# Performance work log

Hardware: AMD Instinct MI355X
Metric: run time of the kernel (lower is better)

## Reference

```python
import jax, jax.numpy as jnp
import numpy as np

N_NODES, N_EDGES, N_PAIRS, FEAT, N_LAYERS = 10000, 160000, 8, 64, 2


def setup_inputs() -> dict:
    key = jax.random.key(0)
    ks = jax.random.split(key, 12)
    s = 1.0 / np.sqrt(FEAT)
    x = jax.random.normal(ks[0], (N_NODES, FEAT), jnp.float32)
    # distinct node ids so unique(pos) has exactly 2*N_PAIRS elements (static B)
    pos = jax.random.permutation(ks[1], N_NODES)[: 2 * N_PAIRS].reshape(N_PAIRS, 2).astype(jnp.int32)
    edge_src = jax.random.randint(ks[2], (N_EDGES,), 0, N_NODES, jnp.int32)
    edge_dst = jax.random.randint(ks[3], (N_EDGES,), 0, N_NODES, jnp.int32)
    edge_weight = jax.random.uniform(ks[4], (N_EDGES,), jnp.float32)
    f0_w = jax.random.normal(ks[5], (N_LAYERS, FEAT, FEAT), jnp.float32) * s
    f0_b = jax.random.normal(ks[6], (N_LAYERS, FEAT), jnp.float32) * 0.01
    f1_w = jax.random.normal(ks[7], (N_LAYERS, FEAT, FEAT), jnp.float32) * s
    f1_b = jax.random.normal(ks[8], (N_LAYERS, FEAT), jnp.float32) * 0.01
    conv_w = jax.random.normal(ks[9], (N_LAYERS, FEAT, FEAT), jnp.float32) * s
    conv_b = jax.random.normal(ks[10], (N_LAYERS, FEAT), jnp.float32) * 0.01
    return {"x": x, "pos": pos, "edge_src": edge_src, "edge_dst": edge_dst,
            "edge_weight": edge_weight, "f0_w": f0_w, "f0_b": f0_b,
            "f1_w": f1_w, "f1_b": f1_b, "conv_w": conv_w, "conv_b": conv_b}


def reference(x, pos, edge_src, edge_dst, edge_weight, f0_w, f0_b, f1_w, f1_b, conv_w, conv_b):
    N = x.shape[0]
    M = pos.shape[0]
    B = 2 * M  # pos entries are distinct -> B unique labeled nodes (static)
    L = f0_w.shape[0]
    # convert_pos: sel_id = unique labeled nodes, ret = flat index into (B*N)
    sel_id, inv = jnp.unique(pos, return_inverse=True, size=B, fill_value=0)
    inv = inv.reshape(pos.shape)
    ret = pos + inv[:, ::-1] * N  # (M,2): pair (u,v) -> x0[batch_of_v, u], x0[batch_of_u, v]
    idx0 = jnp.arange(B)

    h = x  # layer 0: (N,F); later layers: (B,N,H)
    for i in range(L):
        if i == 0:
            base = h @ f0_w[0] + f0_b[0]                         # (N,H)
            x0 = jnp.broadcast_to(base, (B,) + base.shape)       # (B,N,H)
            x1 = h[sel_id] @ f1_w[0] + f1_b[0]                   # (B,H)
        else:
            x0 = h @ f0_w[i] + f0_b[i]                           # (B,N,H)
            x1 = h[idx0, sel_id] @ f1_w[i] + f1_b[i]             # (B,H)
        x0 = x0.at[idx0, sel_id].set(x1)  # scatter labeled-node embeddings
        # sparse adjacency conv: aggregate over edges, then linear
        xT = jnp.swapaxes(x0, 0, 1)                              # (N,B,H)
        msgs = xT[edge_src] * edge_weight[:, None, None]         # (E,B,H)
        agg = jax.ops.segment_sum(msgs, edge_dst, num_segments=N)  # (N,B,H)
        h = jnp.swapaxes(agg, 0, 1) @ conv_w[i] + conv_b[i]      # (B,N,H)
        if i < L - 1:
            h = jax.nn.relu(h)
    flat = h.reshape(B * N, -1)
    return flat[ret]  # (M, 2, H)
```

## Files before the change

kernel.cpp:

```cpp
#include <hip/hip_runtime.h>

#define F 64
#define SECAP 8192
#define TCAP 2048

__global__ __launch_bounds__(256) void k0_init(const int* __restrict__ pos, int B,
                                               int4* __restrict__ z0, int nz0_vec,
                                               int* __restrict__ sel,
                                               int* __restrict__ slotb,
                                               int* __restrict__ slotn) {
  int bid = blockIdx.x, tid = threadIdx.x;
  int i = bid * 256 + tid;
  if (i < nz0_vec) z0[i] = make_int4(0, 0, 0, 0);
  if (bid == (int)gridDim.x - 1) {
    __shared__ int ps[64];
    if (tid < B) ps[tid] = pos[tid];
    __syncthreads();
    if (tid < B) {
      int v = ps[tid];
      int pv = ps[tid ^ 1];
      int rank = 0, pr = 0;
      for (int j = 0; j < B; ++j) { rank += (ps[j] < v); pr += (ps[j] < pv); }
      sel[rank] = v;
      slotb[tid] = pr;
      slotn[tid] = v;
    }
  }
}

__global__ __launch_bounds__(256) void k23_main(
    const float* __restrict__ x, const float* __restrict__ f0w,
    const float* __restrict__ f0b, float* __restrict__ base0, int N,
    const int* __restrict__ esrc, const int* __restrict__ edst,
    const float* __restrict__ ew, int E, int B,
    const int* __restrict__ sel, const int* __restrict__ slotn,
    int* __restrict__ cnt, int* __restrict__ mark, int* __restrict__ slot_of,
    int* __restrict__ SEb, int* __restrict__ SEd, float* __restrict__ SEw,
    int* __restrict__ TEn, int* __restrict__ TEsrc2, float* __restrict__ TEw2,
    int4* __restrict__ z1, int nz1_vec, int nG, int nE) {
  int bid = blockIdx.x, tid = threadIdx.x;
  if (bid < nG) {
    __shared__ float Wl[64][64];
    __shared__ float xr[4][64];
    int tx = tid & 63, ty = tid >> 6;
    for (int i = tid; i < 4096; i += 256) Wl[i >> 6][i & 63] = f0w[i];
    int row = bid * 4 + ty;
    if (row < N) xr[ty][tx] = x[(size_t)row * F + tx];
    __syncthreads();
    if (row < N) {
      float sum = f0b[tx];
#pragma unroll
      for (int f = 0; f < 64; ++f) sum += xr[ty][f] * Wl[f][tx];
      base0[(size_t)row * F + tx] = sum;
    }
  } else if (bid < nG + nE) {
    int ebi = bid - nG;
    __shared__ int selL[64], tnL[64];
    if (tid < B) { selL[tid] = sel[tid]; tnL[tid] = slotn[tid]; }
    __syncthreads();
    if (ebi == 0 && tid < B) {
      int n = selL[tid];
      int old = atomicAdd(&mark[n], 1);
      if (old == 0) slot_of[n] = atomicAdd(&cnt[2], 1);
    }
    int e = ebi * 256 + tid;
    if (e < E) {
      int s = esrc[e], d = edst[e];
      float w = ew[e];
      int bi = -1, ti = -1;
      for (int i = 0; i < B; ++i) {
        if (s == selL[i]) bi = i;
        if (d == tnL[i]) ti = i;
      }
      if (bi >= 0) {
        int idx = atomicAdd(&cnt[0], 1);
        if (idx < SECAP) { SEb[idx] = bi; SEd[idx] = d; SEw[idx] = w; }
      }
      if (ti >= 0) {
        int idx = atomicAdd(&TEn[ti], 1);
        if (idx < TCAP) { TEsrc2[ti * TCAP + idx] = s; TEw2[ti * TCAP + idx] = w; }
        int old = atomicAdd(&mark[s], 1);
        if (old == 0) slot_of[s] = atomicAdd(&cnt[2], 1);
      }
    }
  } else {
    int i = (bid - nG - nE) * 256 + tid;
    if (i < nz1_vec) z1[i] = make_int4(0, 0, 0, 0);
  }
}

__global__ __launch_bounds__(256) void k4b_agg(const int* __restrict__ esrc,
                                               const int* __restrict__ edst,
                                               const float* __restrict__ ew, int E,
                                               const int* __restrict__ mark,
                                               const int* __restrict__ slot_of,
                                               const float* __restrict__ base0,
                                               float* __restrict__ AGG, int fcap) {
  int e = blockIdx.x * 256 + threadIdx.x;
  if (e >= E) return;
  int d = edst[e];
  if (mark[d] == 0) return;
  int slot = slot_of[d];
  if ((unsigned)slot >= (unsigned)fcap) return;
  int s = esrc[e];
  float w = ew[e];
  const float4* src4 = (const float4*)(base0 + (size_t)s * F);
  float* dst = AGG + (size_t)slot * F;
#pragma unroll
  for (int i = 0; i < 16; ++i) {
    float4 v = src4[i];
    atomicAdd(dst + 4 * i + 0, w * v.x);
    atomicAdd(dst + 4 * i + 1, w * v.y);
    atomicAdd(dst + 4 * i + 2, w * v.z);
    atomicAdd(dst + 4 * i + 3, w * v.w);
  }
}

__global__ __launch_bounds__(256) void k55b(
    const float* __restrict__ AGG, const float* __restrict__ cw,
    const float* __restrict__ cb, float* __restrict__ zf,
    const int* __restrict__ cnt, int fcap,
    const int* __restrict__ SEb, const int* __restrict__ SEd,
    const float* __restrict__ SEw,
    const int* __restrict__ mark, const int* __restrict__ slot_of,
    float* __restrict__ ctab,
    const int* __restrict__ TEn, const int* __restrict__ TEsrc2,
    const int* __restrict__ sel, const int* __restrict__ slotb,
    int* __restrict__ TEslot2, int B, int nA, int nB_) {
  int bid = blockIdx.x, tid = threadIdx.x;
  if (bid < nA) {
    int ty = tid >> 6, h = tid & 63;
    int slot = bid * 4 + ty;
    int Fn = min(cnt[2], fcap);
    if (slot >= Fn) return;
    __shared__ float a[4][64];
    a[ty][h] = AGG[(size_t)slot * F + h];
    float sum = cb[h];
#pragma unroll
    for (int f = 0; f < 64; ++f) sum += a[ty][f] * cw[f * 64 + h];
    zf[(size_t)slot * F + h] = sum;
  } else if (bid < nA + nB_) {
    int i = (bid - nA) * 256 + tid;
    int sen = min(cnt[0], SECAP);
    if (i >= sen) return;
    int d = SEd[i];
    if (mark[d] == 0) return;
    int slot = slot_of[d];
    if ((unsigned)slot >= (unsigned)fcap) return;
    atomicAdd(&ctab[(size_t)SEb[i] * fcap + slot], SEw[i]);
  } else {
    int idx = (bid - nA - nB_) * 256 + tid;
    int t = idx / TCAP, i = idx % TCAP;
    if (t >= B) return;
    int n = min(TEn[t], TCAP);
    if (i >= n) return;
    int s = TEsrc2[t * TCAP + i];
    int b = slotb[t];
    int ts;
    if (s == sel[b]) {
      ts = -1;
    } else {
      ts = slot_of[s];
      if ((unsigned)ts >= (unsigned)fcap) ts = 0;
    }
    TEslot2[t * TCAP + i] = ts;
  }
}

__global__ __launch_bounds__(64) void k7_final(
    const int* __restrict__ slotb, const int* __restrict__ sel,
    const int* __restrict__ slot_of,
    const float* __restrict__ x, const float* __restrict__ base0,
    const float* __restrict__ f1w, const float* __restrict__ f1b,
    const float* __restrict__ f0w, const float* __restrict__ f0b,
    const float* __restrict__ cw, const float* __restrict__ cb,
    const float* __restrict__ zf, const float* __restrict__ ctab,
    const int* __restrict__ TEn, const int* __restrict__ TEslot2,
    const float* __restrict__ TEw2,
    float* __restrict__ out, int fcap) {
  int t = blockIdx.x, h = threadIdx.x;
  int b = slotb[t];
  int seln = sel[b];
  __shared__ float sh[64];
  __shared__ int esl[TCAP];
  __shared__ float ewl[TCAP];
  int ten = min(TEn[t], TCAP);
  for (int i = h; i < ten; i += 64) {
    esl[i] = TEslot2[t * TCAP + i];
    ewl[i] = TEw2[t * TCAP + i];
  }
  sh[h] = x[(size_t)seln * F + h];
  __syncthreads();
  float acc = f1b[h];
#pragma unroll
  for (int f = 0; f < 64; ++f) acc += sh[f] * f1w[f * 64 + h];
  float d0h = acc - base0[(size_t)seln * F + h];
  __syncthreads();
  sh[h] = d0h;
  __syncthreads();
  float g0h = 0.f;
#pragma unroll
  for (int f = 0; f < 64; ++f) g0h += sh[f] * cw[f * 64 + h];
  int sslot = slot_of[seln];
  if ((unsigned)sslot >= (unsigned)fcap) sslot = 0;
  float cself = ctab[(size_t)b * fcap + sslot];
  float h1self = fmaxf(zf[(size_t)sslot * F + h] + cself * g0h, 0.f);
  __syncthreads();
  sh[h] = h1self;
  __syncthreads();
  float x11h = f1b[64 + h];
#pragma unroll
  for (int f = 0; f < 64; ++f) x11h += sh[f] * f1w[4096 + f * 64 + h];
  float S = 0.f, wns = 0.f, wsel = 0.f;
  for (int i = 0; i < ten; ++i) {
    int slot = esl[i];
    float w = ewl[i];
    if (slot < 0) { wsel += w; continue; }
    float c = ctab[(size_t)b * fcap + slot];
    float h1 = fmaxf(zf[(size_t)slot * F + h] + c * g0h, 0.f);
    S += w * h1;
    wns += w;
  }
  __syncthreads();
  sh[h] = S;
  __syncthreads();
  float a2 = wns * f0b[64 + h] + wsel * x11h;
#pragma unroll
  for (int f = 0; f < 64; ++f) a2 += sh[f] * f0w[4096 + f * 64 + h];
  __syncthreads();
  sh[h] = a2;
  __syncthreads();
  float o = cb[64 + h];
#pragma unroll
  for (int f = 0; f < 64; ++f) o += sh[f] * cw[4096 + f * 64 + h];
  out[t * F + h] = o;
}

struct Layout {
  size_t cnt, mark, ten, z0_end,
      agg, ctab, z1_end,
      sel, slotb, slotn, slotof,
      seb, sed, sew, tesrc, tew, teslot,
      base0, zf, total;
};

static Layout make_layout(int N, int B, int fcap) {
  Layout L;
  size_t off = 0;
  auto take = [&](size_t nb) {
    size_t r = off;
    off += (nb + 255) & ~(size_t)255;
    return r;
  };
  L.cnt = take(256);
  L.mark = take((size_t)N * 4);
  L.ten = take(256);
  L.z0_end = off;
  L.agg = take((size_t)fcap * F * 4);
  L.ctab = take((size_t)B * fcap * 4);
  L.z1_end = off;
  L.sel = take(256);
  L.slotb = take(256);
  L.slotn = take(256);
  L.slotof = take((size_t)N * 4);
  L.seb = take(SECAP * 4);
  L.sed = take(SECAP * 4);
  L.sew = take(SECAP * 4);
  L.tesrc = take((size_t)B * TCAP * 4);
  L.tew = take((size_t)B * TCAP * 4);
  L.teslot = take((size_t)B * TCAP * 4);
  L.base0 = take((size_t)N * F * 4);
  L.zf = take((size_t)fcap * F * 4);
  L.total = off;
  return L;
}

extern "C" void kernel_launch(void* const* d_in, const int* in_sizes, int n_in,
                              void* d_out, int out_size, void* d_ws, size_t ws_size,
                              hipStream_t stream) {
  const float* x = (const float*)d_in[0];
  const int* pos = (const int*)d_in[1];
  const int* esrc = (const int*)d_in[2];
  const int* edst = (const int*)d_in[3];
  const float* ew = (const float*)d_in[4];
  const float* f0w = (const float*)d_in[5];
  const float* f0b = (const float*)d_in[6];
  const float* f1w = (const float*)d_in[7];
  const float* f1b = (const float*)d_in[8];
  const float* cw = (const float*)d_in[9];
  const float* cb = (const float*)d_in[10];
  float* out = (float*)d_out;

  const int N = in_sizes[0] / F;
  const int B = in_sizes[1];
  const int E = in_sizes[2];

  int fcap = 8192 + 64;
  Layout L = make_layout(N, B, fcap);
  while (L.total > ws_size && fcap > 272) {
    fcap = fcap / 2 + 64;
    L = make_layout(N, B, fcap);
  }

  char* w = (char*)d_ws;
  int* cnt = (int*)(w + L.cnt);
  int* mark = (int*)(w + L.mark);
  int* TEn = (int*)(w + L.ten);
  float* AGG = (float*)(w + L.agg);
  float* ctab = (float*)(w + L.ctab);
  int* sel = (int*)(w + L.sel);
  int* slotb = (int*)(w + L.slotb);
  int* slotn = (int*)(w + L.slotn);
  int* slotof = (int*)(w + L.slotof);
  int* SEb = (int*)(w + L.seb);
  int* SEd = (int*)(w + L.sed);
  float* SEw = (float*)(w + L.sew);
  int* TEsrc2 = (int*)(w + L.tesrc);
  float* TEw2 = (float*)(w + L.tew);
  int* TEslot2 = (int*)(w + L.teslot);
  float* base0 = (float*)(w + L.base0);
  float* zf = (float*)(w + L.zf);

  int nz0_vec = (int)(L.z0_end / 16);
  int nz0b = (nz0_vec + 255) / 256;
  k0_init<<<nz0b + 1, 256, 0, stream>>>(pos, B, (int4*)w, nz0_vec, sel, slotb, slotn);

  int nG = (N + 3) / 4;
  int nE = (E + 255) / 256;
  int nz1_vec = (int)((L.z1_end - L.agg) / 16);
  int nZ = (nz1_vec + 255) / 256;
  k23_main<<<nG + nE + nZ, 256, 0, stream>>>(
      x, f0w, f0b, base0, N, esrc, edst, ew, E, B, sel, slotn,
      cnt, mark, slotof, SEb, SEd, SEw, TEn, TEsrc2, TEw2,
      (int4*)(w + L.agg), nz1_vec, nG, nE);

  k4b_agg<<<nE, 256, 0, stream>>>(esrc, edst, ew, E, mark, slotof, base0, AGG, fcap);

  int nA = (fcap + 3) / 4;
  int nB_ = SECAP / 256;
  int nC = (B * TCAP + 255) / 256;
  k55b<<<nA + nB_ + nC, 256, 0, stream>>>(AGG, cw, cb, zf, cnt, fcap,
                                          SEb, SEd, SEw, mark, slotof, ctab,
                                          TEn, TEsrc2, sel, slotb, TEslot2, B, nA, nB_);

  k7_final<<<B, 64, 0, stream>>>(slotb, sel, slotof, x, base0, f1w, f1b,
                                 f0w, f0b, cw, cb, zf, ctab, TEn, TEslot2, TEw2,
                                 out, fcap);
  (void)n_in; (void)out_size;
}
```

Measured before the change: 61.46 us.

## Fuse all phases into one cooperative persistent kernel and drop base0 GEMM

Replaces the five launches with one cooperative grid kernel that separates phases with grid syncs, falling back to per-phase kernels if the cooperative launch fails. Layer-0 aggregation now runs directly on x and accumulates a per-slot weight sum, so the dense N×64 base0 GEMM is replaced by applying f0w per frontier slot (linearity of the sparse aggregation). The final per-pair kernel folds f1w minus f0w into one matmul and removes __syncthreads. This cuts launch overhead and the full-graph projection, but grid syncs and a smaller persistent grid may limit parallelism. The removed block barriers around shared-memory reuse in phase 4 look like a race.

```diff
diff --git a/kernel.cpp b/kernel.cpp
--- a/kernel.cpp
+++ b/kernel.cpp
@@ -1,350 +1,295 @@
 #include <hip/hip_runtime.h>
+#include <hip/hip_cooperative_groups.h>
+
+namespace cg = cooperative_groups;
 
 #define F 64
 #define SECAP 8192
 #define TCAP 2048
-
-__global__ __launch_bounds__(256) void k0_init(const int* __restrict__ pos, int B,
-                                               int4* __restrict__ z0, int nz0_vec,
-                                               int* __restrict__ sel,
-                                               int* __restrict__ slotb,
-                                               int* __restrict__ slotn) {
-  int bid = blockIdx.x, tid = threadIdx.x;
-  int i = bid * 256 + tid;
-  if (i < nz0_vec) z0[i] = make_int4(0, 0, 0, 0);
-  if (bid == (int)gridDim.x - 1) {
-    __shared__ int ps[64];
-    if (tid < B) ps[tid] = pos[tid];
-    __syncthreads();
-    if (tid < B) {
-      int v = ps[tid];
-      int pv = ps[tid ^ 1];
-      int rank = 0, pr = 0;
-      for (int j = 0; j < B; ++j) { rank += (ps[j] < v); pr += (ps[j] < pv); }
-      sel[rank] = v;
-      slotb[tid] = pr;
-      slotn[tid] = v;
-    }
-  }
-}
-
-__global__ __launch_bounds__(256) void k23_main(
-    const float* __restrict__ x, const float* __restrict__ f0w,
-    const float* __restrict__ f0b, float* __restrict__ base0, int N,
-    const int* __restrict__ esrc, const int* __restrict__ edst,
-    const float* __restrict__ ew, int E, int B,
-    const int* __restrict__ sel, const int* __restrict__ slotn,
-    int* __restrict__ cnt, int* __restrict__ mark, int* __restrict__ slot_of,
-    int* __restrict__ SEb, int* __restrict__ SEd, float* __restrict__ SEw,
-    int* __restrict__ TEn, int* __restrict__ TEsrc2, float* __restrict__ TEw2,
-    int4* __restrict__ z1, int nz1_vec, int nG, int nE) {
-  int bid = blockIdx.x, tid = threadIdx.x;
-  if (bid < nG) {
-    __shared__ float Wl[64][64];
-    __shared__ float xr[4][64];
-    int tx = tid & 63, ty = tid >> 6;
-    for (int i = tid; i < 4096; i += 256) Wl[i >> 6][i & 63] = f0w[i];
-    int row = bid * 4 + ty;
-    if (row < N) xr[ty][tx] = x[(size_t)row * F + tx];
-    __syncthreads();
-    if (row < N) {
-      float sum = f0b[tx];
-#pragma unroll
-      for (int f = 0; f < 64; ++f) sum += xr[ty][f] * Wl[f][tx];
-      base0[(size_t)row * F + tx] = sum;
-    }
-  } else if (bid < nG + nE) {
-    int ebi = bid - nG;
-    __shared__ int selL[64], tnL[64];
-    if (tid < B) { selL[tid] = sel[tid]; tnL[tid] = slotn[tid]; }
-    __syncthreads();
-    if (ebi == 0 && tid < B) {
-      int n = selL[tid];
-      int old = atomicAdd(&mark[n], 1);
-      if (old == 0) slot_of[n] = atomicAdd(&cnt[2], 1);
-    }
-    int e = ebi * 256 + tid;
-    if (e < E) {
-      int s = esrc[e], d = edst[e];
-      float w = ew[e];
-      int bi = -1, ti = -1;
-      for (int i = 0; i < B; ++i) {
-        if (s == selL[i]) bi = i;
-        if (d == tnL[i]) ti = i;
+#define FCAP 8256
+#define BLK 256
+
+struct Params {
+  const float *x, *ew, *f0w, *f0b, *f1w, *f1b, *cw, *cb;
+  const int *pos, *esrc, *edst;
+  float *out;
+  int B, E;
+  int *cnt, *mark, *TEn, *sel, *slotb, *slotn, *slot_of, *SEb, *SEd, *TEsrc2, *TEslot2;
+  float *SEw, *TEw2, *AGG, *wsum, *ctab, *zf;
+  int4 *zbase;
+  int nzvec;
+};
+
+__device__ __forceinline__ void phase0(const Params& p) {
+  int gtid = blockIdx.x * blockDim.x + threadIdx.x;
+  int nthr = gridDim.x * blockDim.x;
+  for (int i = gtid; i < p.nzvec; i += nthr) p.zbase[i] = make_int4(0, 0, 0, 0);
+  if (blockIdx.x == 0 && threadIdx.x < p.B) {
+    int tid = threadIdx.x;
+    int v = p.pos[tid], pv = p.pos[tid ^ 1];
+    int rank = 0, pr = 0;
+    for (int j = 0; j < p.B; ++j) { int pj = p.pos[j]; rank += (pj < v); pr += (pj < pv); }
+    p.sel[rank] = v;
+    p.slotb[tid] = pr;
+    p.slotn[tid] = v;
+  }
+}
+
+__device__ __forceinline__ void phase1(const Params& p) {
+  __shared__ int selL[64], tnL[64];
+  int tid = threadIdx.x;
+  int B = p.B;
+  if (tid < B) { selL[tid] = p.sel[tid]; tnL[tid] = p.slotn[tid]; }
+  __syncthreads();
+  if (blockIdx.x == 0 && tid < B) {
+    int n = selL[tid];
+    if (atomicAdd(&p.mark[n], 1) == 0) p.slot_of[n] = atomicAdd(&p.cnt[2], 1);
+  }
+  int gtid = blockIdx.x * blockDim.x + tid;
+  int nthr = gridDim.x * blockDim.x;
+  for (int e = gtid; e < p.E; e += nthr) {
+    int s = p.esrc[e], d = p.edst[e];
+    float w = p.ew[e];
+    int bi = -1, ti = -1;
+    for (int i = 0; i < B; ++i) {
+      if (s == selL[i]) bi = i;
+      if (d == tnL[i]) ti = i;
+    }
+    if (bi >= 0) {
+      int idx = atomicAdd(&p.cnt[0], 1);
+      if (idx < SECAP) { p.SEb[idx] = bi; p.SEd[idx] = d; p.SEw[idx] = w; }
+    }
+    if (ti >= 0) {
+      int idx = atomicAdd(&p.TEn[ti], 1);
+      if (idx < TCAP) { p.TEsrc2[ti * TCAP + idx] = s; p.TEw2[ti * TCAP + idx] = w; }
+      if (atomicAdd(&p.mark[s], 1) == 0) p.slot_of[s] = atomicAdd(&p.cnt[2], 1);
+    }
+  }
+}
+
+__device__ __forceinline__ void phase2(const Params& p) {
+  int gtid = blockIdx.x * blockDim.x + threadIdx.x;
+  int nthr = gridDim.x * blockDim.x;
+  int E = p.E, B = p.B;
+  int sen = min(p.cnt[0], SECAP);
+  int total2 = E + sen + B * TCAP;
+  for (int i = gtid; i < total2; i += nthr) {
+    if (i < E) {
+      int d = p.edst[i];
+      if (p.mark[d] != 0) {
+        int slot = p.slot_of[d];
+        if ((unsigned)slot < (unsigned)FCAP) {
+          int s = p.esrc[i];
+          float w = p.ew[i];
+          const float4* xs = (const float4*)(p.x + (size_t)s * F);
+          float* dst = p.AGG + (size_t)slot * F;
+#pragma unroll
+          for (int k = 0; k < 16; ++k) {
+            float4 v = xs[k];
+            atomicAdd(dst + 4 * k + 0, w * v.x);
+            atomicAdd(dst + 4 * k + 1, w * v.y);
+            atomicAdd(dst + 4 * k + 2, w * v.z);
+            atomicAdd(dst + 4 * k + 3, w * v.w);
+          }
+          atomicAdd(&p.wsum[slot], w);
+        }
       }
-      if (bi >= 0) {
-        int idx = atomicAdd(&cnt[0], 1);
-        if (idx < SECAP) { SEb[idx] = bi; SEd[idx] = d; SEw[idx] = w; }
+    } else if (i < E + sen) {
+      int j = i - E;
+      int d = p.SEd[j];
+      if (p.mark[d] != 0) {
+        int slot = p.slot_of[d];
+        if ((unsigned)slot < (unsigned)FCAP)
+          atomicAdd(&p.ctab[(size_t)p.SEb[j] * FCAP + slot], p.SEw[j]);
       }
-      if (ti >= 0) {
-        int idx = atomicAdd(&TEn[ti], 1);
-        if (idx < TCAP) { TEsrc2[ti * TCAP + idx] = s; TEw2[ti * TCAP + idx] = w; }
-        int old = atomicAdd(&mark[s], 1);
-        if (old == 0) slot_of[s] = atomicAdd(&cnt[2], 1);
+    } else {
+      int j = i - E - sen;
+      int t = j / TCAP, k = j - t * TCAP;
+      if (t < B && k < min(p.TEn[t], TCAP)) {
+        int s = p.TEsrc2[t * TCAP + k];
+        int ts;
+        if (s == p.sel[p.slotb[t]]) ts = -1;
+        else { ts = p.slot_of[s]; if ((unsigned)ts >= (unsigned)FCAP) ts = 0; }
+        p.TEslot2[t * TCAP + k] = ts;
       }
     }
-  } else {
-    int i = (bid - nG - nE) * 256 + tid;
-    if (i < nz1_vec) z1[i] = make_int4(0, 0, 0, 0);
-  }
-}
-
-__global__ __launch_bounds__(256) void k4b_agg(const int* __restrict__ esrc,
-                                               const int* __restrict__ edst,
-                                               const float* __restrict__ ew, int E,
-                                               const int* __restrict__ mark,
-                                               const int* __restrict__ slot_of,
-                                               const float* __restrict__ base0,
-                                               float* __restrict__ AGG, int fcap) {
-  int e = blockIdx.x * 256 + threadIdx.x;
-  if (e >= E) return;
-  int d = edst[e];
-  if (mark[d] == 0) return;
-  int slot = slot_of[d];
-  if ((unsigned)slot >= (unsigned)fcap) return;
-  int s = esrc[e];
-  float w = ew[e];
-  const float4* src4 = (const float4*)(base0 + (size_t)s * F);
-  float* dst = AGG + (size_t)slot * F;
-#pragma unroll
-  for (int i = 0; i < 16; ++i) {
-    float4 v = src4[i];
-    atomicAdd(dst + 4 * i + 0, w * v.x);
-    atomicAdd(dst + 4 * i + 1, w * v.y);
-    atomicAdd(dst + 4 * i + 2, w * v.z);
-    atomicAdd(dst + 4 * i + 3, w * v.w);
-  }
-}
-
-__global__ __launch_bounds__(256) void k55b(
-    const float* __restrict__ AGG, const float* __restrict__ cw,
-    const float* __restrict__ cb, float* __restrict__ zf,
-    const int* __restrict__ cnt, int fcap,
-    const int* __restrict__ SEb, const int* __restrict__ SEd,
-    const float* __restrict__ SEw,
-    const int* __restrict__ mark, const int* __restrict__ slot_of,
-    float* __restrict__ ctab,
-    const int* __restrict__ TEn, const int* __restrict__ TEsrc2,
-    const int* __restrict__ sel, const int* __restrict__ slotb,
-    int* __restrict__ TEslot2, int B, int nA, int nB_) {
-  int bid = blockIdx.x, tid = threadIdx.x;
-  if (bid < nA) {
-    int ty = tid >> 6, h = tid & 63;
-    int slot = bid * 4 + ty;
-    int Fn = min(cnt[2], fcap);
-    if (slot >= Fn) return;
-    __shared__ float a[4][64];
-    a[ty][h] = AGG[(size_t)slot * F + h];
-    float sum = cb[h];
-#pragma unroll
-    for (int f = 0; f < 64; ++f) sum += a[ty][f] * cw[f * 64 + h];
-    zf[(size_t)slot * F + h] = sum;
-  } else if (bid < nA + nB_) {
-    int i = (bid - nA) * 256 + tid;
-    int sen = min(cnt[0], SECAP);
-    if (i >= sen) return;
-    int d = SEd[i];
-    if (mark[d] == 0) return;
-    int slot = slot_of[d];
-    if ((unsigned)slot >= (unsigned)fcap) return;
-    atomicAdd(&ctab[(size_t)SEb[i] * fcap + slot], SEw[i]);
-  } else {
-    int idx = (bid - nA - nB_) * 256 + tid;
-    int t = idx / TCAP, i = idx % TCAP;
-    if (t >= B) return;
-    int n = min(TEn[t], TCAP);
-    if (i >= n) return;
-    int s = TEsrc2[t * TCAP + i];
-    int b = slotb[t];
-    int ts;
-    if (s == sel[b]) {
-      ts = -1;
-    } else {
-      ts = slot_of[s];
-      if ((unsigned)ts >= (unsigned)fcap) ts = 0;
-    }
-    TEslot2[t * TCAP + i] = ts;
-  }
-}
-
-__global__ __launch_bounds__(64) void k7_final(
-    const int* __restrict__ slotb, const int* __restrict__ sel,
-    const int* __restrict__ slot_of,
-    const float* __restrict__ x, const float* __restrict__ base0,
-    const float* __restrict__ f1w, const float* __restrict__ f1b,
-    const float* __restrict__ f0w, const float* __restrict__ f0b,
-    const float* __restrict__ cw, const float* __restrict__ cb,
-    const float* __restrict__ zf, const float* __restrict__ ctab,
-    const int* __restrict__ TEn, const int* __restrict__ TEslot2,
-    const float* __restrict__ TEw2,
-    float* __restrict__ out, int fcap) {
+  }
+}
+
+__device__ __forceinline__ void phase3(const Params& p) {
+  __shared__ float a3[4][64], t3[4][64];
+  int Fn = min(p.cnt[2], FCAP);
+  int tid = threadIdx.x;
+  int ty = tid >> 6, h = tid & 63;
+  for (int slot = blockIdx.x * 4 + ty; slot < Fn; slot += gridDim.x * 4) {
+    a3[ty][h] = p.AGG[(size_t)slot * F + h];
+    float acc = p.wsum[slot] * p.f0b[h];
+#pragma unroll
+    for (int f = 0; f < 64; ++f) acc += a3[ty][f] * p.f0w[f * 64 + h];
+    t3[ty][h] = acc;
+    float z = p.cb[h];
+#pragma unroll
+    for (int f = 0; f < 64; ++f) z += t3[ty][f] * p.cw[f * 64 + h];
+    p.zf[(size_t)slot * F + h] = z;
+  }
+}
+
+__device__ __forceinline__ void phase4(const Params& p) {
   int t = blockIdx.x, h = threadIdx.x;
-  int b = slotb[t];
-  int seln = sel[b];
+  if (t >= p.B || h >= 64) return;
   __shared__ float sh[64];
   __shared__ int esl[TCAP];
   __shared__ float ewl[TCAP];
-  int ten = min(TEn[t], TCAP);
+  int b = p.slotb[t];
+  int seln = p.sel[b];
+  int ten = min(p.TEn[t], TCAP);
   for (int i = h; i < ten; i += 64) {
-    esl[i] = TEslot2[t * TCAP + i];
-    ewl[i] = TEw2[t * TCAP + i];
-  }
-  sh[h] = x[(size_t)seln * F + h];
-  __syncthreads();
-  float acc = f1b[h];
-#pragma unroll
-  for (int f = 0; f < 64; ++f) acc += sh[f] * f1w[f * 64 + h];
-  float d0h = acc - base0[(size_t)seln * F + h];
-  __syncthreads();
-  sh[h] = d0h;
-  __syncthreads();
+    esl[i] = p.TEslot2[t * TCAP + i];
+    ewl[i] = p.TEw2[t * TCAP + i];
+  }
+  sh[h] = p.x[(size_t)seln * F + h];
+  float acc = p.f1b[h] - p.f0b[h];
+#pragma unroll
+  for (int f = 0; f < 64; ++f) acc += sh[f] * (p.f1w[f * 64 + h] - p.f0w[f * 64 + h]);
+  sh[h] = acc;
   float g0h = 0.f;
 #pragma unroll
-  for (int f = 0; f < 64; ++f) g0h += sh[f] * cw[f * 64 + h];
-  int sslot = slot_of[seln];
-  if ((unsigned)sslot >= (unsigned)fcap) sslot = 0;
-  float cself = ctab[(size_t)b * fcap + sslot];
-  float h1self = fmaxf(zf[(size_t)sslot * F + h] + cself * g0h, 0.f);
-  __syncthreads();
+  for (int f = 0; f < 64; ++f) g0h += sh[f] * p.cw[f * 64 + h];
+  int sslot = p.slot_of[seln];
+  if ((unsigned)sslot >= (unsigned)FCAP) sslot = 0;
+  float cself = p.ctab[(size_t)b * FCAP + sslot];
+  float h1self = fmaxf(p.zf[(size_t)sslot * F + h] + cself * g0h, 0.f);
   sh[h] = h1self;
-  __syncthreads();
-  float x11h = f1b[64 + h];
-#pragma unroll
-  for (int f = 0; f < 64; ++f) x11h += sh[f] * f1w[4096 + f * 64 + h];
+  float x11h = p.f1b[64 + h];
+#pragma unroll
+  for (int f = 0; f < 64; ++f) x11h += sh[f] * p.f1w[4096 + f * 64 + h];
   float S = 0.f, wns = 0.f, wsel = 0.f;
   for (int i = 0; i < ten; ++i) {
     int slot = esl[i];
     float w = ewl[i];
     if (slot < 0) { wsel += w; continue; }
-    float c = ctab[(size_t)b * fcap + slot];
-    float h1 = fmaxf(zf[(size_t)slot * F + h] + c * g0h, 0.f);
+    float c = p.ctab[(size_t)b * FCAP + slot];
+    float h1 = fmaxf(p.zf[(size_t)slot * F + h] + c * g0h, 0.f);
     S += w * h1;
     wns += w;
   }
-  __syncthreads();
   sh[h] = S;
-  __syncthreads();
-  float a2 = wns * f0b[64 + h] + wsel * x11h;
-#pragma unroll
-  for (int f = 0; f < 64; ++f) a2 += sh[f] * f0w[4096 + f * 64 + h];
-  __syncthreads();
+  float a2 = wns * p.f0b[64 + h] + wsel * x11h;
+#pragma unroll
+  for (int f = 0; f < 64; ++f) a2 += sh[f] * p.f0w[4096 + f * 64 + h];
   sh[h] = a2;
-  __syncthreads();
-  float o = cb[64 + h];
-#pragma unroll
-  for (int f = 0; f < 64; ++f) o += sh[f] * cw[4096 + f * 64 + h];
-  out[t * F + h] = o;
-}
-
-struct Layout {
-  size_t cnt, mark, ten, z0_end,
-      agg, ctab, z1_end,
-      sel, slotb, slotn, slotof,
-      seb, sed, sew, tesrc, tew, teslot,
-      base0, zf, total;
-};
-
-static Layout make_layout(int N, int B, int fcap) {
-  Layout L;
-  size_t off = 0;
-  auto take = [&](size_t nb) {
-    size_t r = off;
-    off += (nb + 255) & ~(size_t)255;
-    return r;
-  };
-  L.cnt = take(256);
-  L.mark = take((size_t)N * 4);
-  L.ten = take(256);
-  L.z0_end = off;
-  L.agg = take((size_t)fcap * F * 4);
-  L.ctab = take((size_t)B * fcap * 4);
-  L.z1_end = off;
-  L.sel = take(256);
-  L.slotb = take(256);
-  L.slotn = take(256);
-  L.slotof = take((size_t)N * 4);
-  L.seb = take(SECAP * 4);
-  L.sed = take(SECAP * 4);
-  L.sew = take(SECAP * 4);
-  L.tesrc = take((size_t)B * TCAP * 4);
-  L.tew = take((size_t)B * TCAP * 4);
-  L.teslot = take((size_t)B * TCAP * 4);
-  L.base0 = take((size_t)N * F * 4);
-  L.zf = take((size_t)fcap * F * 4);
-  L.total = off;
-  return L;
-}
+  float o = p.cb[64 + h];
+#pragma unroll
+  for (int f = 0; f < 64; ++f) o += sh[f] * p.cw[4096 + f * 64 + h];
+  p.out[t * F + h] = o;
+}
+
+__global__ __launch_bounds__(BLK, 2) void fused_all(Params p) {
+  cg::grid_group g = cg::this_grid();
+  phase0(p); g.sync();
+  phase1(p); g.sync();
+  phase2(p); g.sync();
+  phase3(p); g.sync();
+  phase4(p);
+}
+
+__global__ __launch_bounds__(BLK) void kp0(Params p) { phase0(p); }
+__global__ __launch_bounds__(BLK) void kp1(Params p) { phase1(p); }
+__global__ __launch_bounds__(BLK) void kp2(Params p) { phase2(p); }
+__global__ __launch_bounds__(BLK) void kp3(Params p) { phase3(p); }
+__global__ __launch_bounds__(64)  void kp4(Params p) { phase4(p); }
 
 extern "C" void kernel_launch(void* const* d_in, const int* in_sizes, int n_in,
                               void* d_out, int out_size, void* d_ws, size_t ws_size,
                               hipStream_t stream) {
-  const float* x = (const float*)d_in[0];
-  const int* pos = (const int*)d_in[1];
-  const int* esrc = (const int*)d_in[2];
-  const int* edst = (const int*)d_in[3];
-  const float* ew = (const float*)d_in[4];
-  const float* f0w = (const float*)d_in[5];
-  const float* f0b = (const float*)d_in[6];
-  const float* f1w = (const float*)d_in[7];
-  const float* f1b = (const float*)d_in[8];
-  const float* cw = (const float*)d_in[9];
-  const float* cb = (const float*)d_in[10];
-  float* out = (float*)d_out;
-
+  Params hp;
+  hp.x = (const float*)d_in[0];
+  hp.pos = (const int*)d_in[1];
+  hp.esrc = (const int*)d_in[2];
+  hp.edst = (const int*)d_in[3];
+  hp.ew = (const float*)d_in[4];
+  hp.f0w = (const float*)d_in[5];
+  hp.f0b = (const float*)d_in[6];
+  hp.f1w = (const float*)d_in[7];
+  hp.f1b = (const float*)d_in[8];
+  hp.cw = (const float*)d_in[9];
+  hp.cb = (const float*)d_in[10];
+  hp.out = (float*)d_out;
   const int N = in_sizes[0] / F;
-  const int B = in_sizes[1];
-  const int E = in_sizes[2];
-
-  int fcap = 8192 + 64;
-  Layout L = make_layout(N, B, fcap);
-  while (L.total > ws_size && fcap > 272) {
-    fcap = fcap / 2 + 64;
-    L = make_layout(N, B, fcap);
-  }
+  hp.B = in_sizes[1];
+  hp.E = in_sizes[2];
 
   char* w = (char*)d_ws;
-  int* cnt = (int*)(w + L.cnt);
-  int* mark = (int*)(w + L.mark);
-  int* TEn = (int*)(w + L.ten);
-  float* AGG = (float*)(w + L.agg);
-  float* ctab = (float*)(w + L.ctab);
-  int* sel = (int*)(w + L.sel);
-  int* slotb = (int*)(w + L.slotb);
-  int* slotn = (int*)(w + L.slotn);
-  int* slotof = (int*)(w + L.slotof);
-  int* SEb = (int*)(w + L.seb);
-  int* SEd = (int*)(w + L.sed);
-  float* SEw = (float*)(w + L.sew);
-  int* TEsrc2 = (int*)(w + L.tesrc);
-  float* TEw2 = (float*)(w + L.tew);
-  int* TEslot2 = (int*)(w + L.teslot);
-  float* base0 = (float*)(w + L.base0);
-  float* zf = (float*)(w + L.zf);
-
-  int nz0_vec = (int)(L.z0_end / 16);
-  int nz0b = (nz0_vec + 255) / 256;
-  k0_init<<<nz0b + 1, 256, 0, stream>>>(pos, B, (int4*)w, nz0_vec, sel, slotb, slotn);
-
-  int nG = (N + 3) / 4;
-  int nE = (E + 255) / 256;
-  int nz1_vec = (int)((L.z1_end - L.agg) / 16);
-  int nZ = (nz1_vec + 255) / 256;
-  k23_main<<<nG + nE + nZ, 256, 0, stream>>>(
-      x, f0w, f0b, base0, N, esrc, edst, ew, E, B, sel, slotn,
-      cnt, mark, slotof, SEb, SEd, SEw, TEn, TEsrc2, TEw2,
-      (int4*)(w + L.agg), nz1_vec, nG, nE);
-
-  k4b_agg<<<nE, 256, 0, stream>>>(esrc, edst, ew, E, mark, slotof, base0, AGG, fcap);
-
-  int nA = (fcap + 3) / 4;
-  int nB_ = SECAP / 256;
-  int nC = (B * TCAP + 255) / 256;
-  k55b<<<nA + nB_ + nC, 256, 0, stream>>>(AGG, cw, cb, zf, cnt, fcap,
-                                          SEb, SEd, SEw, mark, slotof, ctab,
-                                          TEn, TEsrc2, sel, slotb, TEslot2, B, nA, nB_);
-
-  k7_final<<<B, 64, 0, stream>>>(slotb, sel, slotof, x, base0, f1w, f1b,
-                                 f0w, f0b, cw, cb, zf, ctab, TEn, TEslot2, TEw2,
-                                 out, fcap);
+  size_t off = 0;
+  auto take = [&](size_t nb) { size_t r = off; off += (nb + 255) & ~(size_t)255; return r; };
+  size_t o_cnt = take(256);
+  size_t o_mark = take((size_t)N * 4);
+  size_t o_ten = take(256);
+  size_t o_agg = take((size_t)FCAP * F * 4);
+  size_t o_wsum = take((size_t)FCAP * 4);
+  size_t o_ctab = take((size_t)hp.B * FCAP * 4);
+  size_t zero_end = off;
+  size_t o_sel = take(256);
+  size_t o_slotb = take(256);
+  size_t o_slotn = take(256);
+  size_t o_slotof = take((size_t)N * 4);
+  size_t o_seb = take(SECAP * 4);
+  size_t o_sed = take(SECAP * 4);
+  size_t o_sew = take(SECAP * 4);
+  size_t o_tesrc = take((size_t)hp.B * TCAP * 4);
+  size_t o_tew = take((size_t)hp.B * TCAP * 4);
+  size_t o_teslot = take((size_t)hp.B * TCAP * 4);
+  size_t o_zf = take((size_t)FCAP * F * 4);
+  (void)ws_size;
+
+  hp.cnt = (int*)(w + o_cnt);
+  hp.mark = (int*)(w + o_mark);
+  hp.TEn = (int*)(w + o_ten);
+  hp.AGG = (float*)(w + o_agg);
+  hp.wsum = (float*)(w + o_wsum);
+  hp.ctab = (float*)(w + o_ctab);
+  hp.sel = (int*)(w + o_sel);
+  hp.slotb = (int*)(w + o_slotb);
+  hp.slotn = (int*)(w + o_slotn);
+  hp.slot_of = (int*)(w + o_slotof);
+  hp.SEb = (int*)(w + o_seb);
+  hp.SEd = (int*)(w + o_sed);
+  hp.SEw = (float*)(w + o_sew);
+  hp.TEsrc2 = (int*)(w + o_tesrc);
+  hp.TEw2 = (float*)(w + o_tew);
+  hp.TEslot2 = (int*)(w + o_teslot);
+  hp.zf = (float*)(w + o_zf);
+  hp.zbase = (int4*)w;
+  hp.nzvec = (int)(zero_end / 16);
+
+  int dev = 0;
+  (void)hipGetDevice(&dev);
+  int numCU = 0;
+  (void)hipDeviceGetAttribute(&numCU, hipDeviceAttributeMultiprocessorCount, dev);
+  int maxB = 0;
+  (void)hipOccupancyMaxActiveBlocksPerMultiprocessor(&maxB, (const void*)fused_all, BLK, 0);
+  long long coopGrid = (long long)maxB * (long long)(numCU > 0 ? numCU : 0);
+  if (coopGrid > 624) coopGrid = 624;
+  if (coopGrid >= 64) {
+    void* args[] = { &hp };
+    hipError_t e = hipLaunchCooperativeKernel((const void*)fused_all,
+                                              dim3((unsigned)coopGrid), dim3(BLK),
+                                              args, 0, stream);
+    if (e == hipSuccess) { (void)n_in; (void)out_size; return; }
+    (void)hipGetLastError();
+  }
+
+  int nb0 = (hp.nzvec + BLK - 1) / BLK;
+  if (nb0 < 1) nb0 = 1;
+  if (nb0 > 2048) nb0 = 2048;
+  kp0<<<nb0, BLK, 0, stream>>>(hp);
+  int nb1 = (hp.E + BLK - 1) / BLK;
+  if (nb1 > 2048) nb1 = 2048;
+  kp1<<<nb1, BLK, 0, stream>>>(hp);
+  int nb2 = (hp.E + SECAP + hp.B * TCAP + BLK - 1) / BLK;
+  if (nb2 > 2048) nb2 = 2048;
+  kp2<<<nb2, BLK, 0, stream>>>(hp);
+  kp3<<<512, BLK, 0, stream>>>(hp);
+  kp4<<<hp.B, 64, 0, stream>>>(hp);
   (void)n_in; (void)out_size;
 }
```

Result: slower. 201.3 us (+227.6%).
